# Kernel optimization log

Hardware: AMD Instinct MI355X
Metric: run time of the kernel (lower is better)

The kernel has to match this reference:

```python
import jax, jax.numpy as jnp
import numpy as np
import math

N_WIRES = 8

def _cnot(state, ctrl, tgt):
    # state: (N, 2,2,...,2) with wire w on axis 1+w
    c_ax = 1 + ctrl
    t_ax = 1 + tgt
    s0 = jnp.take(state, 0, axis=c_ax)
    s1 = jnp.take(state, 1, axis=c_ax)
    t2 = t_ax - 1 if t_ax > c_ax else t_ax
    s1 = jnp.flip(s1, axis=t2)
    return jnp.stack([s0, s1], axis=c_ax)

def _qlayer(x, phi):
    # x: (N, 8) encoder RX angles; phi: (8,) trainable RX angles.
    # encoder RX(x_i) followed by RX(phi_i) on the same wire == RX(x_i + phi_i)
    N = x.shape[0]
    half = 0.5 * (x + phi)
    c = jnp.cos(half).astype(jnp.complex64)
    s = jnp.sin(half).astype(jnp.complex64)
    amp = jnp.stack([c, (-1j) * s], axis=-1)  # (N, 8, 2) per-wire RX|0>
    # product state via successive outer products -> (N, 2,...,2)
    state = amp[:, 0]
    for w in range(1, N_WIRES):
        q = amp[:, w].reshape((N,) + (1,) * w + (2,))
        state = state[..., None] * q
    # CNOT ring
    for w in range(N_WIRES - 1):
        state = _cnot(state, w, w + 1)
    state = _cnot(state, N_WIRES - 1, 0)
    probs = state.real ** 2 + state.imag ** 2  # (N, 2,...,2)
    exps = []
    for w in range(N_WIRES):
        axes = tuple(a for a in range(1, N_WIRES + 1) if a != 1 + w)
        pw = jnp.sum(probs, axis=axes)  # (N, 2)
        exps.append(pw[:, 0] - pw[:, 1])  # <Z_w>
    return jnp.stack(exps, axis=-1)  # (N, 8)


def setup_inputs() -> dict:
    key = jax.random.key(0)
    k1, k2, k3 = jax.random.split(key, 3)
    B, S, E = 4, 1024, 128
    x = jax.random.normal(k1, (B, S, E), jnp.float32)
    phi = jax.random.normal(k2, (N_WIRES,), jnp.float32)
    W = jax.random.normal(k3, (E, E), jnp.float32) / math.sqrt(E)
    b = jnp.zeros((E,), jnp.float32)
    return {"x": x, "phi": phi, "W": W, "b": b}


def reference(x, phi, W, b):
    B, S, E = x.shape
    H = 16
    d = N_WIRES  # head dim == n_wires == 8
    xh = x.reshape(B, S, H, d).reshape(-1, d)
    proj = _qlayer(xh, phi).reshape(B, S, H, d)
    # q, k, v are identical (same layer, same input, deterministic) -> compute once
    q = jnp.transpose(proj, (0, 2, 1, 3))  # (B, H, S, d)
    scores = jnp.einsum('bhqd,bhkd->bhqk', q, q) / math.sqrt(d)
    attn = jax.nn.softmax(scores, axis=-1)  # dropout: eval mode (identity)
    out = jnp.einsum('bhqk,bhkd->bhqd', attn, q)
    out = jnp.transpose(out, (0, 2, 1, 3)).reshape(B, S, E)
    return out @ W.T + b
```

## Files before the change

kernel.cpp:

```cpp
#include <hip/hip_runtime.h>

#define NB 4
#define NS 1024
#define NE 128
#define NH 16
#define ND 8

typedef __attribute__((ext_vector_type(4))) _Float16 half4v;
typedef __attribute__((ext_vector_type(8))) _Float16 half8v;
typedef __attribute__((ext_vector_type(2))) _Float16 half2v;
typedef __attribute__((ext_vector_type(4))) float float4v;

#if __has_builtin(__builtin_amdgcn_exp2f)
#define EXP2F(x) __builtin_amdgcn_exp2f(x)
#else
#define EXP2F(x) __expf(0.69314718055994531f * (x))
#endif

#define SQRT_ALPHA 0.71423656f

#define MFMA16(A, B, C) __builtin_amdgcn_mfma_f32_16x16x16f16((A), (B), (C), 0, 0, 0)
#define MFMA32(A, B, C) __builtin_amdgcn_mfma_f32_16x16x32_f16((A), (B), (C), 0, 0, 0)

static __device__ __forceinline__ half8v cat8(half4v lo, half4v hi) {
    return __builtin_shufflevector(lo, hi, 0, 1, 2, 3, 4, 5, 6, 7);
}
static __device__ __forceinline__ half4v cat4(half2v lo, half2v hi) {
    return __builtin_shufflevector(lo, hi, 0, 1, 2, 3);
}

__global__ __launch_bounds__(1024, 8)
void qattn_kernel(const float* __restrict__ x, const float* __restrict__ phi,
                  float* __restrict__ aout)
{
    __shared__ __align__(16) _Float16 KA[NS * 12];
    __shared__ __align__(16) _Float16 Vt[9][1036];
    __shared__ __align__(16) float4 scratch[2][4][2][64];

    const int t    = threadIdx.x;
    const int blk  = blockIdx.x;
    const int qt   = blk & 7;
    const int bh   = blk >> 3;
    const int b    = bh >> 4;
    const int h    = bh & 15;
    const int lane = t & 63;
    const int w    = t >> 6;
    const int qg   = w & 3;
    const int kh   = w >> 2;

    {
        const int k = t;
        const float* xr = x + ((size_t)(b * NS + k)) * NE + h * ND;
        float4 xa = *(const float4*)xr;
        float4 xc = *(const float4*)(xr + 4);
        float g0 = __cosf(xa.x + phi[0]), g1 = __cosf(xa.y + phi[1]);
        float g2 = __cosf(xa.z + phi[2]), g3 = __cosf(xa.w + phi[3]);
        float g4 = __cosf(xc.x + phi[4]), g5 = __cosf(xc.y + phi[5]);
        float g6 = __cosf(xc.z + phi[6]), g7 = __cosf(xc.w + phi[7]);
        float s7 = g7, s6 = s7 * g6, s5 = s6 * g5, s4 = s5 * g4, s3 = s4 * g3, s2 = s3 * g2;
        float v0 = s2 * g1;
        float v1 = g0 * g1, v2 = v1 * g2, v3 = v2 * g3;
        float v4 = v3 * g4, v5 = v4 * g5, v6 = v5 * g6, v7 = v6 * g7;
        half4v rlo, rhi;
        rlo[0] = (_Float16)(SQRT_ALPHA * v0); rlo[1] = (_Float16)(SQRT_ALPHA * v1);
        rlo[2] = (_Float16)(SQRT_ALPHA * v2); rlo[3] = (_Float16)(SQRT_ALPHA * v3);
        rhi[0] = (_Float16)(SQRT_ALPHA * v4); rhi[1] = (_Float16)(SQRT_ALPHA * v5);
        rhi[2] = (_Float16)(SQRT_ALPHA * v6); rhi[3] = (_Float16)(SQRT_ALPHA * v7);
        *(half4v*)&KA[k * 12]     = rlo;
        *(half4v*)&KA[k * 12 + 4] = rhi;
        Vt[0][k] = (_Float16)v0; Vt[1][k] = (_Float16)v1;
        Vt[2][k] = (_Float16)v2; Vt[3][k] = (_Float16)v3;
        Vt[4][k] = (_Float16)v4; Vt[5][k] = (_Float16)v5;
        Vt[6][k] = (_Float16)v6; Vt[7][k] = (_Float16)v7;
        Vt[8][k] = (_Float16)1.0f;
    }
    __syncthreads();

    const int e = lane & 15;
    const int g = lane >> 4;

    half4v qf0 = (half4v)(_Float16)0.0f;
    half4v qf1 = (half4v)(_Float16)0.0f;
    if (lane < 32) {
        const int qrow = qt * 128 + qg * 32 + e;
        qf0 = *(const half4v*)&KA[qrow * 12 + g * 4];
        qf1 = *(const half4v*)&KA[(qrow + 16) * 12 + g * 4];
    }

    const _Float16* kp = &KA[(kh * 256 + e) * 12 + (g & 1) * 4];
    const int ecl = (e > 8) ? 8 : e;
    const _Float16* vp = &Vt[ecl][kh * 256 + g * 4];

    float4v acc0 = (float4v)0.0f;
    float4v acc1 = (float4v)0.0f;
    const float4v zero = (float4v)0.0f;

#pragma unroll 1
    for (int p = 0; p < 8; ++p) {
        const _Float16* kpp = kp + p * 384;
        const _Float16* vpp = vp + p * 32;

        half4v kf0 = *(const half4v*)(kpp);
        half4v kf1 = *(const half4v*)(kpp + 192);
        half4v vf0 = *(const half4v*)(vpp);
        half4v vf1 = *(const half4v*)(vpp + 16);

        float4v s00 = MFMA16(kf0, qf0, zero);
        float4v s01 = MFMA16(kf0, qf1, zero);
        float4v s10 = MFMA16(kf1, qf0, zero);
        float4v s11 = MFMA16(kf1, qf1, zero);

        float p000 = EXP2F(s00[0]), p001 = EXP2F(s00[1]), p002 = EXP2F(s00[2]), p003 = EXP2F(s00[3]);
        float p010 = EXP2F(s01[0]), p011 = EXP2F(s01[1]), p012 = EXP2F(s01[2]), p013 = EXP2F(s01[3]);
        float p100 = EXP2F(s10[0]), p101 = EXP2F(s10[1]), p102 = EXP2F(s10[2]), p103 = EXP2F(s10[3]);
        float p110 = EXP2F(s11[0]), p111 = EXP2F(s11[1]), p112 = EXP2F(s11[2]), p113 = EXP2F(s11[3]);

        half4v paA0 = cat4(__builtin_bit_cast(half2v, __builtin_amdgcn_cvt_pkrtz(p000, p001)),
                           __builtin_bit_cast(half2v, __builtin_amdgcn_cvt_pkrtz(p002, p003)));
        half4v paA1 = cat4(__builtin_bit_cast(half2v, __builtin_amdgcn_cvt_pkrtz(p010, p011)),
                           __builtin_bit_cast(half2v, __builtin_amdgcn_cvt_pkrtz(p012, p013)));
        half4v paB0 = cat4(__builtin_bit_cast(half2v, __builtin_amdgcn_cvt_pkrtz(p100, p101)),
                           __builtin_bit_cast(half2v, __builtin_amdgcn_cvt_pkrtz(p102, p103)));
        half4v paB1 = cat4(__builtin_bit_cast(half2v, __builtin_amdgcn_cvt_pkrtz(p110, p111)),
                           __builtin_bit_cast(half2v, __builtin_amdgcn_cvt_pkrtz(p112, p113)));

        half8v vf8 = cat8(vf0, vf1);
        acc0 = MFMA32(cat8(paA0, paB0), vf8, acc0);
        acc1 = MFMA32(cat8(paA1, paB1), vf8, acc1);
    }

    if (kh >= 2) {
        scratch[kh - 2][qg][0][lane] = make_float4(acc0[0], acc0[1], acc0[2], acc0[3]);
        scratch[kh - 2][qg][1][lane] = make_float4(acc1[0], acc1[1], acc1[2], acc1[3]);
    }
    __syncthreads();
    if (kh < 2) {
        float4 c0 = scratch[kh][qg][0][lane];
        float4 c1 = scratch[kh][qg][1][lane];
        acc0[0] += c0.x; acc0[1] += c0.y; acc0[2] += c0.z; acc0[3] += c0.w;
        acc1[0] += c1.x; acc1[1] += c1.y; acc1[2] += c1.z; acc1[3] += c1.w;
    }
    if (kh == 1) {
        scratch[1][qg][0][lane] = make_float4(acc0[0], acc0[1], acc0[2], acc0[3]);
        scratch[1][qg][1][lane] = make_float4(acc1[0], acc1[1], acc1[2], acc1[3]);
    }
    __syncthreads();
    if (kh == 0) {
        float4 c0 = scratch[1][qg][0][lane];
        float4 c1 = scratch[1][qg][1][lane];
        acc0[0] += c0.x; acc0[1] += c0.y; acc0[2] += c0.z; acc0[3] += c0.w;
        acc1[0] += c1.x; acc1[1] += c1.y; acc1[2] += c1.z; acc1[3] += c1.w;

        const int src = (lane & 48) | 8;
        const size_t rb = (size_t)(b * NS + qt * 128 + qg * 32 + g * 4);
        float* opb = aout + rb * NE + h * ND + e;
#pragma unroll
        for (int qs = 0; qs < 2; ++qs) {
            float4v a = qs ? acc1 : acc0;
            float d0 = __shfl(a[0], src, 64);
            float d1 = __shfl(a[1], src, 64);
            float d2 = __shfl(a[2], src, 64);
            float d3 = __shfl(a[3], src, 64);
            if (e < 8) {
                float* op = opb + (size_t)(qs * 16) * NE;
                op[0 * NE] = a[0] / d0;
                op[1 * NE] = a[1] / d1;
                op[2 * NE] = a[2] / d2;
                op[3 * NE] = a[3] / d3;
            }
        }
    }
}

__global__ __launch_bounds__(256)
void proj_kernel(const float* __restrict__ A, const float* __restrict__ W,
                 const float* __restrict__ bias, float* __restrict__ out)
{
    __shared__ __align__(16) _Float16 Wh[NE][140];
    __shared__ __align__(16) _Float16 As[16][140];

    const int t  = threadIdx.x;
    const int r0 = blockIdx.x * 16;

    for (int i = t; i < 16 * 32; i += 256) {
        int m = i >> 5, k4 = (i & 31) * 4;
        float4 a4 = *(const float4*)&A[(size_t)(r0 + m) * NE + k4];
        half2v h01 = __builtin_bit_cast(half2v, __builtin_amdgcn_cvt_pkrtz(a4.x, a4.y));
        half2v h23 = __builtin_bit_cast(half2v, __builtin_amdgcn_cvt_pkrtz(a4.z, a4.w));
        *(half4v*)&As[m][k4] = __builtin_shufflevector(h01, h23, 0, 1, 2, 3);
    }
    for (int i = t; i < NE * 32; i += 256) {
        int n = i >> 5, k4 = (i & 31) * 4;
        float4 w4 = *(const float4*)&W[(size_t)n * NE + k4];
        half2v h01 = __builtin_bit_cast(half2v, __builtin_amdgcn_cvt_pkrtz(w4.x, w4.y));
        half2v h23 = __builtin_bit_cast(half2v, __builtin_amdgcn_cvt_pkrtz(w4.z, w4.w));
        *(half4v*)&Wh[n][k4] = __builtin_shufflevector(h01, h23, 0, 1, 2, 3);
    }
    __syncthreads();

    const int lane = t & 63;
    const int wv   = t >> 6;
    const int e    = lane & 15;
    const int g    = lane >> 4;

    float4v acc0 = (float4v)0.0f;
    float4v acc1 = (float4v)0.0f;

#pragma unroll
    for (int c = 0; c < 8; ++c) {
        half4v af  = *(const half4v*)&As[e][c * 16 + g * 4];
        half4v bf0 = *(const half4v*)&Wh[wv * 32 + e][c * 16 + g * 4];
        half4v bf1 = *(const half4v*)&Wh[wv * 32 + 16 + e][c * 16 + g * 4];
        acc0 = __builtin_amdgcn_mfma_f32_16x16x16f16(af, bf0, acc0, 0, 0, 0);
        acc1 = __builtin_amdgcn_mfma_f32_16x16x16f16(af, bf1, acc1, 0, 0, 0);
    }

    const float bv0 = bias[wv * 32 + e];
    const float bv1 = bias[wv * 32 + 16 + e];
    float* ob = out + (size_t)(r0 + g * 4) * NE + wv * 32 + e;
#pragma unroll
    for (int r = 0; r < 4; ++r) {
        ob[(size_t)r * NE]      = acc0[r] + bv0;
        ob[(size_t)r * NE + 16] = acc1[r] + bv1;
    }
}

extern "C" void kernel_launch(void* const* d_in, const int* in_sizes, int n_in,
                              void* d_out, int out_size, void* d_ws, size_t ws_size,
                              hipStream_t stream)
{
    (void)in_sizes; (void)n_in; (void)out_size; (void)d_ws; (void)ws_size;
    const float* x   = (const float*)d_in[0];
    const float* phi = (const float*)d_in[1];
    const float* W   = (const float*)d_in[2];
    const float* b   = (const float*)d_in[3];
    float* out = (float*)d_out;

    qattn_kernel<<<dim3(NB * NH * 8), dim3(1024), 0, stream>>>(x, phi, out);
    proj_kernel<<<dim3(NB * NS / 16), dim3(256), 0, stream>>>(out, W, b, out);
}
```

Measured before the change: 20.88 us.

## Precompute quantum layer features once in a separate kernel instead of per block

Before, each of the 8 query-tile blocks per (batch, head) recomputed the cosine products for all 1024 keys, reading strided x rows from global memory. A new kernel computes the scaled fp16 feature rows once into workspace in (b,h,s) order. The attention kernel then loads those contiguous rows and rebuilds V by multiplying by the inverse scale in fp16. This removes 8x redundant transcendental work and the strided loads, at the cost of an extra launch, a global round trip through workspace, and slight extra fp16 rounding in V.

```diff
diff --git a/kernel.cpp b/kernel.cpp
--- a/kernel.cpp
+++ b/kernel.cpp
@@ -18,6 +18,7 @@
 #endif
 
 #define SQRT_ALPHA 0.71423656f
+#define INV_SQRT_ALPHA 1.4000968f
 
 #define MFMA16(A, B, C) __builtin_amdgcn_mfma_f32_16x16x16f16((A), (B), (C), 0, 0, 0)
 #define MFMA32(A, B, C) __builtin_amdgcn_mfma_f32_16x16x32_f16((A), (B), (C), 0, 0, 0)
@@ -29,9 +30,40 @@
     return __builtin_shufflevector(lo, hi, 0, 1, 2, 3);
 }
 
+__global__ __launch_bounds__(256)
+void qlayer_kernel(const float* __restrict__ x, const float* __restrict__ phi,
+                   _Float16* __restrict__ kws)
+{
+    const int tid = blockIdx.x * 256 + threadIdx.x;
+    const int h   = tid & 15;
+    const int bs  = tid >> 4;
+    const int b   = bs >> 10;
+    const int s   = bs & (NS - 1);
+
+    const float* xr = x + (size_t)bs * NE + h * ND;
+    float4 xa = *(const float4*)xr;
+    float4 xc = *(const float4*)(xr + 4);
+    float g0 = __cosf(xa.x + phi[0]), g1 = __cosf(xa.y + phi[1]);
+    float g2 = __cosf(xa.z + phi[2]), g3 = __cosf(xa.w + phi[3]);
+    float g4 = __cosf(xc.x + phi[4]), g5 = __cosf(xc.y + phi[5]);
+    float g6 = __cosf(xc.z + phi[6]), g7 = __cosf(xc.w + phi[7]);
+    float s7 = g7, s6 = s7 * g6, s5 = s6 * g5, s4 = s5 * g4, s3 = s4 * g3, s2 = s3 * g2;
+    float v0 = s2 * g1;
+    float v1 = g0 * g1, v2 = v1 * g2, v3 = v2 * g3;
+    float v4 = v3 * g4, v5 = v4 * g5, v6 = v5 * g6, v7 = v6 * g7;
+
+    half8v row;
+    row[0] = (_Float16)(SQRT_ALPHA * v0); row[1] = (_Float16)(SQRT_ALPHA * v1);
+    row[2] = (_Float16)(SQRT_ALPHA * v2); row[3] = (_Float16)(SQRT_ALPHA * v3);
+    row[4] = (_Float16)(SQRT_ALPHA * v4); row[5] = (_Float16)(SQRT_ALPHA * v5);
+    row[6] = (_Float16)(SQRT_ALPHA * v6); row[7] = (_Float16)(SQRT_ALPHA * v7);
+
+    const size_t idx = ((size_t)((b * NH + h) * NS + s)) * 8;
+    *(half8v*)&kws[idx] = row;
+}
+
 __global__ __launch_bounds__(1024, 8)
-void qattn_kernel(const float* __restrict__ x, const float* __restrict__ phi,
-                  float* __restrict__ aout)
+void qattn_kernel(const _Float16* __restrict__ kws, float* __restrict__ aout)
 {
     __shared__ __align__(16) _Float16 KA[NS * 12];
     __shared__ __align__(16) _Float16 Vt[9][1036];
@@ -41,8 +73,6 @@
     const int blk  = blockIdx.x;
     const int qt   = blk & 7;
     const int bh   = blk >> 3;
-    const int b    = bh >> 4;
-    const int h    = bh & 15;
     const int lane = t & 63;
     const int w    = t >> 6;
     const int qg   = w & 3;
@@ -50,28 +80,12 @@
 
     {
         const int k = t;
-        const float* xr = x + ((size_t)(b * NS + k)) * NE + h * ND;
-        float4 xa = *(const float4*)xr;
-        float4 xc = *(const float4*)(xr + 4);
-        float g0 = __cosf(xa.x + phi[0]), g1 = __cosf(xa.y + phi[1]);
-        float g2 = __cosf(xa.z + phi[2]), g3 = __cosf(xa.w + phi[3]);
-        float g4 = __cosf(xc.x + phi[4]), g5 = __cosf(xc.y + phi[5]);
-        float g6 = __cosf(xc.z + phi[6]), g7 = __cosf(xc.w + phi[7]);
-        float s7 = g7, s6 = s7 * g6, s5 = s6 * g5, s4 = s5 * g4, s3 = s4 * g3, s2 = s3 * g2;
-        float v0 = s2 * g1;
-        float v1 = g0 * g1, v2 = v1 * g2, v3 = v2 * g3;
-        float v4 = v3 * g4, v5 = v4 * g5, v6 = v5 * g6, v7 = v6 * g7;
-        half4v rlo, rhi;
-        rlo[0] = (_Float16)(SQRT_ALPHA * v0); rlo[1] = (_Float16)(SQRT_ALPHA * v1);
-        rlo[2] = (_Float16)(SQRT_ALPHA * v2); rlo[3] = (_Float16)(SQRT_ALPHA * v3);
-        rhi[0] = (_Float16)(SQRT_ALPHA * v4); rhi[1] = (_Float16)(SQRT_ALPHA * v5);
-        rhi[2] = (_Float16)(SQRT_ALPHA * v6); rhi[3] = (_Float16)(SQRT_ALPHA * v7);
-        *(half4v*)&KA[k * 12]     = rlo;
-        *(half4v*)&KA[k * 12 + 4] = rhi;
-        Vt[0][k] = (_Float16)v0; Vt[1][k] = (_Float16)v1;
-        Vt[2][k] = (_Float16)v2; Vt[3][k] = (_Float16)v3;
-        Vt[4][k] = (_Float16)v4; Vt[5][k] = (_Float16)v5;
-        Vt[6][k] = (_Float16)v6; Vt[7][k] = (_Float16)v7;
+        half8v row = *(const half8v*)&kws[((size_t)bh * NS + k) * 8];
+        *(half4v*)&KA[k * 12]     = __builtin_shufflevector(row, row, 0, 1, 2, 3);
+        *(half4v*)&KA[k * 12 + 4] = __builtin_shufflevector(row, row, 4, 5, 6, 7);
+        half8v vr = row * (half8v)(_Float16)INV_SQRT_ALPHA;
+        Vt[0][k] = vr[0]; Vt[1][k] = vr[1]; Vt[2][k] = vr[2]; Vt[3][k] = vr[3];
+        Vt[4][k] = vr[4]; Vt[5][k] = vr[5]; Vt[6][k] = vr[6]; Vt[7][k] = vr[7];
         Vt[8][k] = (_Float16)1.0f;
     }
     __syncthreads();
@@ -151,6 +165,8 @@
         acc0[0] += c0.x; acc0[1] += c0.y; acc0[2] += c0.z; acc0[3] += c0.w;
         acc1[0] += c1.x; acc1[1] += c1.y; acc1[2] += c1.z; acc1[3] += c1.w;
 
+        const int b = bh >> 4;
+        const int h = bh & 15;
         const int src = (lane & 48) | 8;
         const size_t rb = (size_t)(b * NS + qt * 128 + qg * 32 + g * 4);
         float* opb = aout + rb * NE + h * ND + e;
@@ -187,14 +203,14 @@
         float4 a4 = *(const float4*)&A[(size_t)(r0 + m) * NE + k4];
         half2v h01 = __builtin_bit_cast(half2v, __builtin_amdgcn_cvt_pkrtz(a4.x, a4.y));
         half2v h23 = __builtin_bit_cast(half2v, __builtin_amdgcn_cvt_pkrtz(a4.z, a4.w));
-        *(half4v*)&As[m][k4] = __builtin_shufflevector(h01, h23, 0, 1, 2, 3);
+        *(half4v*)&As[m][k4] = cat4(h01, h23);
     }
     for (int i = t; i < NE * 32; i += 256) {
         int n = i >> 5, k4 = (i & 31) * 4;
         float4 w4 = *(const float4*)&W[(size_t)n * NE + k4];
         half2v h01 = __builtin_bit_cast(half2v, __builtin_amdgcn_cvt_pkrtz(w4.x, w4.y));
         half2v h23 = __builtin_bit_cast(half2v, __builtin_amdgcn_cvt_pkrtz(w4.z, w4.w));
-        *(half4v*)&Wh[n][k4] = __builtin_shufflevector(h01, h23, 0, 1, 2, 3);
+        *(half4v*)&Wh[n][k4] = cat4(h01, h23);
     }
     __syncthreads();
 
@@ -211,8 +227,8 @@
         half4v af  = *(const half4v*)&As[e][c * 16 + g * 4];
         half4v bf0 = *(const half4v*)&Wh[wv * 32 + e][c * 16 + g * 4];
         half4v bf1 = *(const half4v*)&Wh[wv * 32 + 16 + e][c * 16 + g * 4];
-        acc0 = __builtin_amdgcn_mfma_f32_16x16x16f16(af, bf0, acc0, 0, 0, 0);
-        acc1 = __builtin_amdgcn_mfma_f32_16x16x16f16(af, bf1, acc1, 0, 0, 0);
+        acc0 = MFMA16(af, bf0, acc0);
+        acc1 = MFMA16(af, bf1, acc1);
     }
 
     const float bv0 = bias[wv * 32 + e];
@@ -229,13 +245,15 @@
                               void* d_out, int out_size, void* d_ws, size_t ws_size,
                               hipStream_t stream)
 {
-    (void)in_sizes; (void)n_in; (void)out_size; (void)d_ws; (void)ws_size;
+    (void)in_sizes; (void)n_in; (void)out_size; (void)ws_size;
     const float* x   = (const float*)d_in[0];
     const float* phi = (const float*)d_in[1];
     const float* W   = (const float*)d_in[2];
     const float* b   = (const float*)d_in[3];
     float* out = (float*)d_out;
-
-    qattn_kernel<<<dim3(NB * NH * 8), dim3(1024), 0, stream>>>(x, phi, out);
+    _Float16* kws = (_Float16*)d_ws;
+
+    qlayer_kernel<<<dim3(NB * NS * NH / 256), dim3(256), 0, stream>>>(x, phi, kws);
+    qattn_kernel<<<dim3(NB * NH * 8), dim3(1024), 0, stream>>>(kws, out);
     proj_kernel<<<dim3(NB * NS / 16), dim3(256), 0, stream>>>(out, W, b, out);
 }
```

Result: slower. 24.86 us (+19.1%).

## Fuse output projection into attention kernel via last-block-done atomic counter

Applied to the files above, without the earlier changes.

Drops the separate projection kernel launch. Each attention block bumps a per-(batch, query-tile) counter after writing its head slice, and the block that arrives sixteenth (the last head) performs the 128x128 output projection for that 128-row tile, with W staged as fp16 in reused shared memory. This removes one kernel launch and the inter-kernel gap but adds a memset, atomics and threadfences, and serializes the projection onto a few last blocks.

```diff
diff --git a/kernel.cpp b/kernel.cpp
--- a/kernel.cpp
+++ b/kernel.cpp
@@ -28,14 +28,20 @@
 static __device__ __forceinline__ half4v cat4(half2v lo, half2v hi) {
     return __builtin_shufflevector(lo, hi, 0, 1, 2, 3);
 }
+static __device__ __forceinline__ half4v cvt4(float4 a) {
+    return cat4(__builtin_bit_cast(half2v, __builtin_amdgcn_cvt_pkrtz(a.x, a.y)),
+                __builtin_bit_cast(half2v, __builtin_amdgcn_cvt_pkrtz(a.z, a.w)));
+}
 
 __global__ __launch_bounds__(1024, 8)
-void qattn_kernel(const float* __restrict__ x, const float* __restrict__ phi,
-                  float* __restrict__ aout)
+void qattn_fused_kernel(const float* __restrict__ x, const float* __restrict__ phi,
+                        const float* __restrict__ W, const float* __restrict__ bias,
+                        float* __restrict__ out, unsigned int* __restrict__ cnt)
 {
     __shared__ __align__(16) _Float16 KA[NS * 12];
     __shared__ __align__(16) _Float16 Vt[9][1036];
     __shared__ __align__(16) float4 scratch[2][4][2][64];
+    __shared__ int elect;
 
     const int t    = threadIdx.x;
     const int blk  = blockIdx.x;
@@ -153,7 +159,7 @@
 
         const int src = (lane & 48) | 8;
         const size_t rb = (size_t)(b * NS + qt * 128 + qg * 32 + g * 4);
-        float* opb = aout + rb * NE + h * ND + e;
+        float* opb = out + rb * NE + h * ND + e;
 #pragma unroll
         for (int qs = 0; qs < 2; ++qs) {
             float4v a = qs ? acc1 : acc0;
@@ -170,58 +176,49 @@
             }
         }
     }
-}
-
-__global__ __launch_bounds__(256)
-void proj_kernel(const float* __restrict__ A, const float* __restrict__ W,
-                 const float* __restrict__ bias, float* __restrict__ out)
-{
-    __shared__ __align__(16) _Float16 Wh[NE][140];
-    __shared__ __align__(16) _Float16 As[16][140];
-
-    const int t  = threadIdx.x;
-    const int r0 = blockIdx.x * 16;
-
-    for (int i = t; i < 16 * 32; i += 256) {
-        int m = i >> 5, k4 = (i & 31) * 4;
-        float4 a4 = *(const float4*)&A[(size_t)(r0 + m) * NE + k4];
-        half2v h01 = __builtin_bit_cast(half2v, __builtin_amdgcn_cvt_pkrtz(a4.x, a4.y));
-        half2v h23 = __builtin_bit_cast(half2v, __builtin_amdgcn_cvt_pkrtz(a4.z, a4.w));
-        *(half4v*)&As[m][k4] = __builtin_shufflevector(h01, h23, 0, 1, 2, 3);
-    }
-    for (int i = t; i < NE * 32; i += 256) {
+
+    __syncthreads();
+    if (t == 0) {
+        __threadfence();
+        elect = (int)atomicAdd(&cnt[b * 8 + qt], 1u);
+    }
+    __syncthreads();
+    if (elect != 15) return;
+
+    __threadfence();
+    _Float16* Wh = (_Float16*)KA;
+
+    for (int i = t; i < NE * 32; i += 1024) {
         int n = i >> 5, k4 = (i & 31) * 4;
-        float4 w4 = *(const float4*)&W[(size_t)n * NE + k4];
-        half2v h01 = __builtin_bit_cast(half2v, __builtin_amdgcn_cvt_pkrtz(w4.x, w4.y));
-        half2v h23 = __builtin_bit_cast(half2v, __builtin_amdgcn_cvt_pkrtz(w4.z, w4.w));
-        *(half4v*)&Wh[n][k4] = __builtin_shufflevector(h01, h23, 0, 1, 2, 3);
-    }
-    __syncthreads();
-
-    const int lane = t & 63;
-    const int wv   = t >> 6;
-    const int e    = lane & 15;
-    const int g    = lane >> 4;
-
-    float4v acc0 = (float4v)0.0f;
-    float4v acc1 = (float4v)0.0f;
-
+        *(half4v*)&Wh[n * 132 + k4] = cvt4(*(const float4*)&W[(size_t)n * NE + k4]);
+    }
+
+    const int r0 = b * NS + qt * 128;
+    const int mt = w >> 1;
+    const int n0 = (w & 1) * 4;
+
+    half4v af[8];
 #pragma unroll
     for (int c = 0; c < 8; ++c) {
-        half4v af  = *(const half4v*)&As[e][c * 16 + g * 4];
-        half4v bf0 = *(const half4v*)&Wh[wv * 32 + e][c * 16 + g * 4];
-        half4v bf1 = *(const half4v*)&Wh[wv * 32 + 16 + e][c * 16 + g * 4];
-        acc0 = __builtin_amdgcn_mfma_f32_16x16x16f16(af, bf0, acc0, 0, 0, 0);
-        acc1 = __builtin_amdgcn_mfma_f32_16x16x16f16(af, bf1, acc1, 0, 0, 0);
-    }
-
-    const float bv0 = bias[wv * 32 + e];
-    const float bv1 = bias[wv * 32 + 16 + e];
-    float* ob = out + (size_t)(r0 + g * 4) * NE + wv * 32 + e;
-#pragma unroll
-    for (int r = 0; r < 4; ++r) {
-        ob[(size_t)r * NE]      = acc0[r] + bv0;
-        ob[(size_t)r * NE + 16] = acc1[r] + bv1;
+        af[c] = cvt4(*(const float4*)&out[(size_t)(r0 + mt * 16 + e) * NE + c * 16 + g * 4]);
+    }
+
+    __syncthreads();
+
+#pragma unroll
+    for (int nt = n0; nt < n0 + 4; ++nt) {
+        float4v pacc = (float4v)0.0f;
+#pragma unroll
+        for (int c = 0; c < 8; ++c) {
+            half4v wf = *(const half4v*)&Wh[(nt * 16 + e) * 132 + c * 16 + g * 4];
+            pacc = MFMA16(af[c], wf, pacc);
+        }
+        const float bv = bias[nt * 16 + e];
+        float* ob = out + (size_t)(r0 + mt * 16 + g * 4) * NE + nt * 16 + e;
+#pragma unroll
+        for (int r = 0; r < 4; ++r) {
+            ob[(size_t)r * NE] = pacc[r] + bv;
+        }
     }
 }
 
@@ -229,13 +226,14 @@
                               void* d_out, int out_size, void* d_ws, size_t ws_size,
                               hipStream_t stream)
 {
-    (void)in_sizes; (void)n_in; (void)out_size; (void)d_ws; (void)ws_size;
+    (void)in_sizes; (void)n_in; (void)out_size; (void)ws_size;
     const float* x   = (const float*)d_in[0];
     const float* phi = (const float*)d_in[1];
     const float* W   = (const float*)d_in[2];
     const float* b   = (const float*)d_in[3];
     float* out = (float*)d_out;
-
-    qattn_kernel<<<dim3(NB * NH * 8), dim3(1024), 0, stream>>>(x, phi, out);
-    proj_kernel<<<dim3(NB * NS / 16), dim3(256), 0, stream>>>(out, W, b, out);
-}
+    unsigned int* cnt = (unsigned int*)d_ws;
+
+    hipMemsetAsync(cnt, 0, 32 * sizeof(unsigned int), stream);
+    qattn_fused_kernel<<<dim3(NB * NH * 8), dim3(1024), 0, stream>>>(x, phi, W, b, out, cnt);
+}
```

After: 49.98 us. 139% more time.
